# Optimization experiments

Hardware: AMD Instinct MI355X
Metric: run time of the kernel (lower is better)

The kernel has to match this reference:

```python
import jax, jax.numpy as jnp
import numpy as np

DIM = 256
HEADS = 8
HEAD_DIM = DIM // HEADS
SCALE = HEAD_DIM ** -0.5
B, H, W = 4, 48, 48


def setup_inputs() -> dict:
    key = jax.random.key(0)
    ks = jax.random.split(key, 10)
    s = 1.0 / np.sqrt(DIM)
    return {
        "img_features": jax.random.normal(ks[0], (B, DIM, H, W), jnp.float32),
        "radar_features": jax.random.normal(ks[1], (B, DIM, H, W), jnp.float32),
        "uncertainty_mask": jax.random.uniform(ks[2], (B, 1, H, W), jnp.float32),
        "Wq_img": jax.random.normal(ks[3], (DIM, DIM), jnp.float32) * s,
        "Wkv_radar": jax.random.normal(ks[4], (DIM, 2 * DIM), jnp.float32) * s,
        "Wq_radar": jax.random.normal(ks[5], (DIM, DIM), jnp.float32) * s,
        "Wkv_img": jax.random.normal(ks[6], (DIM, 2 * DIM), jnp.float32) * s,
        "Wp_img": jax.random.normal(ks[7], (DIM, DIM), jnp.float32) * s,
        "bp_img": jnp.zeros((DIM,), jnp.float32),
        "Wp_radar": jax.random.normal(ks[8], (DIM, DIM), jnp.float32) * s,
        "bp_radar": jnp.zeros((DIM,), jnp.float32),
    }


def _heads(x, b, n):
    # (B, N, C) -> (B, heads, N, head_dim)
    return x.reshape(b, n, HEADS, HEAD_DIM).transpose(0, 2, 1, 3)


def _cross_attn(q_seq, kv_seq, Wq, Wkv, uw=None):
    b, n, c = q_seq.shape
    q = _heads(q_seq @ Wq, b, n)                      # (B,h,N,d)
    kv = (kv_seq @ Wkv).reshape(b, n, 2, HEADS, HEAD_DIM)
    k = kv[:, :, 0].transpose(0, 2, 1, 3)             # (B,h,N,d)
    v = kv[:, :, 1].transpose(0, 2, 1, 3)
    scores = jnp.einsum("bhnd,bhmd->bhnm", q, k) * SCALE
    if uw is not None:
        scores = scores * uw                          # (B,1,N,1) broadcast
    p = jax.nn.softmax(scores, axis=-1)
    out = jnp.einsum("bhnm,bhmd->bhnd", p, v)
    return out.transpose(0, 2, 1, 3).reshape(b, n, c)


def reference(img_features, radar_features, uncertainty_mask,
              Wq_img, Wkv_radar, Wq_radar, Wkv_img,
              Wp_img, bp_img, Wp_radar, bp_radar):
    b, c, h, w = img_features.shape
    n = h * w
    img_seq = img_features.reshape(b, c, n).transpose(0, 2, 1)    # (B,N,C)
    radar_seq = radar_features.reshape(b, c, n).transpose(0, 2, 1)

    # uncertainty weight: (B,1,N,1), scales query rows before softmax
    u_seq = uncertainty_mask.reshape(b, 1, n).transpose(0, 2, 1)  # (B,N,1)
    uw = (1.0 / (u_seq + 1e-6))[:, None, :, :]

    img_att = _cross_attn(img_seq, radar_seq, Wq_img, Wkv_radar, uw)
    img_att = img_att @ Wp_img + bp_img

    radar_att = _cross_attn(radar_seq, img_seq, Wq_radar, Wkv_img, None)
    radar_att = radar_att @ Wp_radar + bp_radar

    img_out = img_att.transpose(0, 2, 1).reshape(b, c, h, w)
    radar_out = radar_att.transpose(0, 2, 1).reshape(b, c, h, w)
    return img_out, radar_out
```

## Files before the change

kernel.cpp:

```cpp
#include <hip/hip_runtime.h>
#include <math.h>

#define NB    4
#define CDIM  256
#define NSEQ  2304
#define NHEAD 8
#define HD    32
#define QSCALE (0.17677669529663687f * 1.4426950408889634f)
#define INV2048 4.8828125e-4f
#define FIXMAX 12.0f

typedef _Float16 f16;
typedef _Float16 f16x8 __attribute__((ext_vector_type(8)));
typedef _Float16 f16x4 __attribute__((ext_vector_type(4)));
typedef _Float16 f16x2 __attribute__((ext_vector_type(2)));
typedef float    f32x4 __attribute__((ext_vector_type(4)));
typedef float    f32x16 __attribute__((ext_vector_type(16)));
typedef unsigned u32x4 __attribute__((ext_vector_type(4)));

__device__ __forceinline__ float fast_exp2(float x) {
#if __has_builtin(__builtin_amdgcn_exp2f)
  return __builtin_amdgcn_exp2f(x);
#else
  return exp2f(x);
#endif
}

__device__ __forceinline__ unsigned pkrtz(float a, float b) {
#if __has_builtin(__builtin_amdgcn_cvt_pkrtz)
  auto h = __builtin_amdgcn_cvt_pkrtz(a, b);
  return __builtin_bit_cast(unsigned, h);
#else
  f16x2 h; h[0] = (f16)a; h[1] = (f16)b;
  return __builtin_bit_cast(unsigned, h);
#endif
}

__device__ __forceinline__ void gload_lds16(const f16* g, f16* l) {
  __builtin_amdgcn_global_load_lds(
      (const __attribute__((address_space(1))) void*)g,
      (__attribute__((address_space(3))) void*)l, 16, 0, 0);
}

__device__ __forceinline__ void plswap(unsigned &a, unsigned &b) {
#if __has_builtin(__builtin_amdgcn_permlane32_swap)
  auto r = __builtin_amdgcn_permlane32_swap(a, b, false, false);
  a = r[0]; b = r[1];
#else
  asm("v_permlane32_swap_b32 %0, %1" : "+v"(a), "+v"(b));
#endif
}

__device__ __forceinline__ float cross_fmax(float v) {
  unsigned a = __builtin_bit_cast(unsigned, v), b;
  asm("v_mov_b32 %0, %1" : "=v"(b) : "v"(a));
  plswap(a, b);
  return fmaxf(__builtin_bit_cast(float, a), __builtin_bit_cast(float, b));
}
__device__ __forceinline__ float cross_add(float v) {
  unsigned a = __builtin_bit_cast(unsigned, v), b;
  asm("v_mov_b32 %0, %1" : "=v"(b) : "v"(a));
  plswap(a, b);
  return __builtin_bit_cast(float, a) + __builtin_bit_cast(float, b);
}

__global__ __launch_bounds__(256) void prep_split(
    const float* __restrict__ X0, const float* __restrict__ X1,
    const float* __restrict__ Wq0, const float* __restrict__ Wkv0,
    const float* __restrict__ Wp0, const float* __restrict__ Wq1,
    const float* __restrict__ Wkv1, const float* __restrict__ Wp1,
    f16* __restrict__ X16h, f16* __restrict__ X16l,
    f16* __restrict__ WTh, f16* __restrict__ WTl)
{
  __shared__ float Ls[64][65];
  const int t = threadIdx.x;
  const int id = blockIdx.x;

  const float* in; int incols, c0, col0; size_t obase; f16 *oh, *ol;
  float scale = 1.f;
  if (id < 1152) {
    int mb = id / 144, rem = id % 144;
    int ct = rem / 36, nt = rem % 36;
    int mod = mb >> 2, b = mb & 3;
    in = (mod ? X1 : X0) + (size_t)b * 256 * NSEQ;
    incols = NSEQ; c0 = ct * 64; col0 = nt * 64;
    obase = (size_t)mb * NSEQ + col0;
    oh = X16h; ol = X16l;
  } else {
    int wid = id - 1152;
    int mod = wid >> 6, r = wid & 63;
    int jt, ct2, rowoff;
    if (r < 16) {
      in = mod ? Wq1 : Wq0; incols = 256; jt = r >> 2; ct2 = r & 3;
      rowoff = 0; scale = QSCALE;
    } else if (r < 48) {
      int rr = r - 16;
      in = mod ? Wkv1 : Wkv0; incols = 512; jt = rr >> 2; ct2 = rr & 3;
      rowoff = 256;
    } else {
      int rr = r - 48;
      in = mod ? Wp1 : Wp0; incols = 256; jt = rr >> 2; ct2 = rr & 3;
      rowoff = 768;
    }
    c0 = ct2 * 64; col0 = jt * 64;
    obase = (size_t)mod * 1024 + rowoff + col0;
    oh = WTh; ol = WTl;
  }

#pragma unroll
  for (int i = 0; i < 4; ++i) {
    int cl = (t >> 4) + i * 16;
    int n4 = (t & 15) * 4;
    *(float4*)&Ls[cl][n4] =
        *(const float4*)(in + (size_t)(c0 + cl) * incols + col0 + n4);
  }
  __syncthreads();
#pragma unroll
  for (int i = 0; i < 4; ++i) {
    int ll = (t >> 4) + i * 16;
    int c4 = (t & 15) * 4;
    f16x4 hv, lv;
#pragma unroll
    for (int j = 0; j < 4; ++j) {
      float v = Ls[c4 + j][ll] * scale;
      f16 hh = (f16)v;
      hv[j] = hh;
      lv[j] = (f16)((v - (float)hh) * 2048.0f);
    }
    size_t o = (obase + ll) * 256 + c0 + c4;
    *(f16x4*)(oh + o) = hv;
    *(f16x4*)(ol + o) = lv;
  }
}

__global__ __launch_bounds__(256) void proj_qkv_mfma(
    const f16* __restrict__ X16h, const f16* __restrict__ X16l,
    const f16* __restrict__ WTh, const f16* __restrict__ WTl,
    f16* __restrict__ Qh, f16* __restrict__ Ql,
    f16* __restrict__ Kh, f16* __restrict__ Kl, f16* __restrict__ Vt)
{
  __shared__ f16 WhS[128][32];
  __shared__ f16 WlS[128][32];
  __shared__ f16 XhS[64][32];
  __shared__ f16 XlS[64][32];

  const int zz = blockIdx.z, mod = zz >> 2, b = zz & 3;
  const int n0 = blockIdx.y * 64, j0 = blockIdx.x * 128;
  const int t = threadIdx.x;
  const int wave = t >> 6, lane = t & 63;
  const int col = lane & 15, quad = lane >> 4;
  const int rsub = lane >> 2, seg8 = (lane & 3) * 8;

  const bool need_lo = (j0 < 256) ? (mod == 0)
                     : (j0 < 512) ? (mod == 1) : false;

  const size_t wbase = (size_t)mod * 1024 + j0;
  const size_t xbase = ((size_t)(mod * NB + b) * NSEQ + n0) * 256;

  f32x4 am[2][4], ac[2][4];
#pragma unroll
  for (int s = 0; s < 2; ++s)
#pragma unroll
    for (int tt = 0; tt < 4; ++tt) {
      am[s][tt] = (f32x4){0.f, 0.f, 0.f, 0.f};
      ac[s][tt] = (f32x4){0.f, 0.f, 0.f, 0.f};
    }

  for (int c0 = 0; c0 < 256; c0 += 32) {
    __syncthreads();
    {
      const f16* gw = WTh + (wbase + wave * 32 + rsub) * 256 + c0 + seg8;
      gload_lds16(gw,            &WhS[wave * 32][0]);
      gload_lds16(gw + 16 * 256, &WhS[wave * 32 + 16][0]);
      const f16* gx = X16h + xbase + (size_t)(wave * 16 + rsub) * 256 + c0 + seg8;
      gload_lds16(gx, &XhS[wave * 16][0]);
      if (need_lo) {
        const f16* gwl = WTl + (wbase + wave * 32 + rsub) * 256 + c0 + seg8;
        gload_lds16(gwl,            &WlS[wave * 32][0]);
        gload_lds16(gwl + 16 * 256, &WlS[wave * 32 + 16][0]);
        const f16* gxl = X16l + xbase + (size_t)(wave * 16 + rsub) * 256 + c0 + seg8;
        gload_lds16(gxl, &XlS[wave * 16][0]);
      }
    }
    __syncthreads();

    f16x8 Ah0 = *(const f16x8*)&WhS[wave * 32 + col][quad * 8];
    f16x8 Ah1 = *(const f16x8*)&WhS[wave * 32 + 16 + col][quad * 8];
    if (need_lo) {
      f16x8 Al0 = *(const f16x8*)&WlS[wave * 32 + col][quad * 8];
      f16x8 Al1 = *(const f16x8*)&WlS[wave * 32 + 16 + col][quad * 8];
#pragma unroll
      for (int tt = 0; tt < 4; ++tt) {
        f16x8 Bh = *(const f16x8*)&XhS[tt * 16 + col][quad * 8];
        f16x8 Bl = *(const f16x8*)&XlS[tt * 16 + col][quad * 8];
        am[0][tt] = __builtin_amdgcn_mfma_f32_16x16x32_f16(Ah0, Bh, am[0][tt], 0, 0, 0);
        ac[0][tt] = __builtin_amdgcn_mfma_f32_16x16x32_f16(Ah0, Bl, ac[0][tt], 0, 0, 0);
        ac[0][tt] = __builtin_amdgcn_mfma_f32_16x16x32_f16(Al0, Bh, ac[0][tt], 0, 0, 0);
        am[1][tt] = __builtin_amdgcn_mfma_f32_16x16x32_f16(Ah1, Bh, am[1][tt], 0, 0, 0);
        ac[1][tt] = __builtin_amdgcn_mfma_f32_16x16x32_f16(Ah1, Bl, ac[1][tt], 0, 0, 0);
        ac[1][tt] = __builtin_amdgcn_mfma_f32_16x16x32_f16(Al1, Bh, ac[1][tt], 0, 0, 0);
      }
    } else {
#pragma unroll
      for (int tt = 0; tt < 4; ++tt) {
        f16x8 Bh = *(const f16x8*)&XhS[tt * 16 + col][quad * 8];
        am[0][tt] = __builtin_amdgcn_mfma_f32_16x16x32_f16(Ah0, Bh, am[0][tt], 0, 0, 0);
        am[1][tt] = __builtin_amdgcn_mfma_f32_16x16x32_f16(Ah1, Bh, am[1][tt], 0, 0, 0);
      }
    }
  }

#pragma unroll
  for (int s = 0; s < 2; ++s) {
    const int jq = j0 + wave * 32 + s * 16 + quad * 4;
#pragma unroll
    for (int tt = 0; tt < 4; ++tt) {
      const int n = n0 + tt * 16 + col;
      float v[4];
#pragma unroll
      for (int r = 0; r < 4; ++r)
        v[r] = need_lo ? fmaf(ac[s][tt][r], INV2048, am[s][tt][r])
                       : am[s][tt][r];
      if (jq < 256) {
        f16x4 hv, lv;
#pragma unroll
        for (int r = 0; r < 4; ++r) {
          f16 hh = (f16)v[r]; hv[r] = hh;
          lv[r] = (f16)(v[r] - (float)hh);
        }
        *(f16x4*)(Qh + ((size_t)(mod * NB + b) * NSEQ + n) * 256 + jq) = hv;
        if (mod == 0)
          *(f16x4*)(Ql + ((size_t)b * NSEQ + n) * 256 + jq) = lv;
      } else if (jq < 512) {
        f16x4 hv, lv;
#pragma unroll
        for (int r = 0; r < 4; ++r) {
          f16 hh = (f16)v[r]; hv[r] = hh;
          lv[r] = (f16)(v[r] - (float)hh);
        }
        *(f16x4*)(Kh + ((size_t)(mod * NB + b) * NSEQ + n) * 256 + (jq - 256)) = hv;
        if (mod == 1)
          *(f16x4*)(Kl + ((size_t)b * NSEQ + n) * 256 + (jq - 256)) = lv;
      } else {
#pragma unroll
        for (int r = 0; r < 4; ++r)
          Vt[((size_t)(mod * NB + b) * 256 + (jq - 512 + r)) * NSEQ + n] = (f16)v[r];
      }
    }
  }
}

__global__ __launch_bounds__(256, 3) void attn_mfma(
    const f16* __restrict__ Qh, const f16* __restrict__ Ql,
    const f16* __restrict__ Kh, const f16* __restrict__ Kl,
    const f16* __restrict__ Vt, const float* __restrict__ U,
    f16* __restrict__ A16)
{
  __shared__ __align__(16) f16 KhS[64][40];
  __shared__ __align__(16) f16 KlS[64][40];
  __shared__ __align__(16) f16 VtS[32][72];

  const int branch = blockIdx.x;
  const int bh = blockIdx.y, b = bh >> 3, h = bh & 7;
  const int tid = threadIdx.x;
  const int wave = tid >> 6, lane = tid & 63;
  const int c32 = lane & 31, hi = lane >> 5;
  const int qr = blockIdx.z * 128 + wave * 32 + c32;

  unsigned da = (lane < 32) ? 1u : 2u;
  unsigned db = (lane < 32) ? 3u : 4u;
  plswap(da, db);
  const bool varA = (__builtin_amdgcn_readfirstlane((int)da) == 1);

  const int qmod = branch, kmod = 1 - branch;
  const size_t qbase = (size_t)(qmod * NB + b) * NSEQ * 256;
  const size_t kbase = (size_t)(kmod * NB + b) * NSEQ;
  const size_t kbaseL = (size_t)b * NSEQ;
  const size_t vbase = (size_t)(kmod * NB + b) * 256;

  f16x8 bqh[2], bql[2] = {};
  bqh[0] = *(const f16x8*)(Qh + qbase + (size_t)qr * 256 + h * HD + hi * 8);
  bqh[1] = *(const f16x8*)(Qh + qbase + (size_t)qr * 256 + h * HD + 16 + hi * 8);
  float uw = 1.0f;
  if (branch == 0) {
    const size_t qbaseL = (size_t)b * NSEQ * 256;
    bql[0] = *(const f16x8*)(Ql + qbaseL + (size_t)qr * 256 + h * HD + hi * 8);
    bql[1] = *(const f16x8*)(Ql + qbaseL + (size_t)qr * 256 + h * HD + 16 + hi * 8);
    uw = 1.0f / (U[b * NSEQ + qr] + 1e-6f);
  }

  float m = -1e30f, l = 0.f;
  f32x16 oc;
#pragma unroll
  for (int r = 0; r < 16; ++r) oc[r] = 0.f;
  f32x16 z16;
#pragma unroll
  for (int r = 0; r < 16; ++r) z16[r] = 0.f;

  const int krow = tid >> 2, kseg = (tid & 3) * 8;
  const int vrow = tid >> 3, vseg = (tid & 7) * 8;

  f16x8 pkh = *(const f16x8*)(Kh + (kbase + krow) * 256 + h * HD + kseg);
  f16x8 pkl = {};
  if (branch == 0)
    pkl = *(const f16x8*)(Kl + (kbaseL + krow) * 256 + h * HD + kseg);
  f16x8 pv = *(const f16x8*)(Vt + (vbase + h * HD + vrow) * NSEQ + vseg);

  for (int k0 = 0; k0 < NSEQ; k0 += 64) {
    __syncthreads();
    *(f16x8*)&KhS[krow][kseg] = pkh;
    if (branch == 0) *(f16x8*)&KlS[krow][kseg] = pkl;
    *(f16x8*)&VtS[vrow][vseg] = pv;
    __syncthreads();

    const int kn = (k0 + 64 < NSEQ) ? k0 + 64 : 0;
    pkh = *(const f16x8*)(Kh + (kbase + kn + krow) * 256 + h * HD + kseg);
    if (branch == 0)
      pkl = *(const f16x8*)(Kl + (kbaseL + kn + krow) * 256 + h * HD + kseg);
    pv = *(const f16x8*)(Vt + (vbase + h * HD + vrow) * NSEQ + kn + vseg);

    float p[2][16];
#pragma unroll
    for (int kt = 0; kt < 2; ++kt) {
      f32x16 acc;
      if (branch == 0) {
        f16x8 ah0 = *(const f16x8*)&KhS[kt * 32 + c32][hi * 8];
        f16x8 ah1 = *(const f16x8*)&KhS[kt * 32 + c32][16 + hi * 8];
        f16x8 al0 = *(const f16x8*)&KlS[kt * 32 + c32][hi * 8];
        f16x8 al1 = *(const f16x8*)&KlS[kt * 32 + c32][16 + hi * 8];
        acc = __builtin_amdgcn_mfma_f32_32x32x16_f16(ah0, bql[0], z16, 0, 0, 0);
        acc = __builtin_amdgcn_mfma_f32_32x32x16_f16(al0, bqh[0], acc, 0, 0, 0);
        acc = __builtin_amdgcn_mfma_f32_32x32x16_f16(ah1, bql[1], acc, 0, 0, 0);
        acc = __builtin_amdgcn_mfma_f32_32x32x16_f16(al1, bqh[1], acc, 0, 0, 0);
        acc = __builtin_amdgcn_mfma_f32_32x32x16_f16(ah0, bqh[0], acc, 0, 0, 0);
        acc = __builtin_amdgcn_mfma_f32_32x32x16_f16(ah1, bqh[1], acc, 0, 0, 0);
      } else {
        f16x8 ah0 = *(const f16x8*)&KhS[kt * 32 + c32][hi * 8];
        f16x8 ah1 = *(const f16x8*)&KhS[kt * 32 + c32][16 + hi * 8];
        acc = __builtin_amdgcn_mfma_f32_32x32x16_f16(ah0, bqh[0], z16, 0, 0, 0);
        acc = __builtin_amdgcn_mfma_f32_32x32x16_f16(ah1, bqh[1], acc, 0, 0, 0);
      }
#pragma unroll
      for (int r = 0; r < 16; ++r) p[kt][r] = acc[r];
    }

    if (branch == 0) {
      float t8[8];
#pragma unroll
      for (int i = 0; i < 8; ++i)
        t8[i] = fmaxf(fmaxf(fmaxf(p[0][i], p[0][i + 8]), p[1][i]), p[1][i + 8]);
#pragma unroll
      for (int s = 4; s > 0; s >>= 1)
#pragma unroll
        for (int i = 0; i < s; ++i) t8[i] = fmaxf(t8[i], t8[i + s]);
      float cmax = cross_fmax(t8[0] * uw);
      const bool nore = __all(cmax <= m);
      const float mn = nore ? m : fmaxf(m, cmax);
      float sA = 0.f, sB = 0.f;
#pragma unroll
      for (int kt = 0; kt < 2; ++kt)
#pragma unroll
        for (int r = 0; r < 16; r += 2) {
          float eA = fast_exp2(fmaf(p[kt][r],     uw, -mn));
          float eB = fast_exp2(fmaf(p[kt][r + 1], uw, -mn));
          p[kt][r] = eA; p[kt][r + 1] = eB;
          sA += eA; sB += eB;
        }
      if (nore) {
        l += sA + sB;
      } else {
        const float alpha = fast_exp2(m - mn);
        m = mn;
        l = fmaf(l, alpha, sA + sB);
#pragma unroll
        for (int r = 0; r < 16; ++r) oc[r] *= alpha;
      }
    } else {
      float sA = 0.f, sB = 0.f;
#pragma unroll
      for (int kt = 0; kt < 2; ++kt)
#pragma unroll
        for (int r = 0; r < 16; r += 2) {
          float eA = fast_exp2(p[kt][r]     - FIXMAX);
          float eB = fast_exp2(p[kt][r + 1] - FIXMAX);
          p[kt][r] = eA; p[kt][r + 1] = eB;
          sA += eA; sB += eB;
        }
      l += sA + sB;
    }

    unsigned pk[2][4][2];
#pragma unroll
    for (int kt = 0; kt < 2; ++kt)
#pragma unroll
      for (int Q = 0; Q < 4; ++Q) {
        pk[kt][Q][0] = pkrtz(p[kt][4 * Q],     p[kt][4 * Q + 1]);
        pk[kt][Q][1] = pkrtz(p[kt][4 * Q + 2], p[kt][4 * Q + 3]);
      }

#pragma unroll
    for (int km = 0; km < 4; ++km) {
      const int kt = km >> 1, Qb = (km & 1) * 2;
      unsigned w0 = pk[kt][Qb][0],     w1 = pk[kt][Qb][1];
      unsigned w2 = pk[kt][Qb + 1][0], w3 = pk[kt][Qb + 1][1];
      if (varA) { plswap(w0, w2); plswap(w1, w3); }
      else      { plswap(w2, w0); plswap(w3, w1); }
      u32x4 uv = {w0, w1, w2, w3};
      f16x8 bp = __builtin_bit_cast(f16x8, uv);
      f16x8 av = *(const f16x8*)&VtS[c32][km * 16 + hi * 8];
      oc = __builtin_amdgcn_mfma_f32_32x32x16_f16(av, bp, oc, 0, 0, 0);
    }
  }

  l = cross_add(l);

  const float iv = 1.0f / l;
  f16* d0 = A16 + (((size_t)(branch * NB + b) * NSEQ) + qr) * 256 + h * HD + hi * 4;
#pragma unroll
  for (int g = 0; g < 4; ++g) {
    f16x4 o;
#pragma unroll
    for (int r = 0; r < 4; ++r) o[r] = (f16)(oc[4 * g + r] * iv);
    *(f16x4*)(d0 + 8 * g) = o;
  }
}

__global__ __launch_bounds__(256) void proj_out_mfma(
    const f16* __restrict__ A16, const f16* __restrict__ WTh,
    const f16* __restrict__ WTl, const float* __restrict__ bp0,
    const float* __restrict__ bp1, float* __restrict__ O)
{
  __shared__ f16 WhS[128][32];
  __shared__ f16 WlS[128][32];
  __shared__ f16 AS[64][32];

  const int zz = blockIdx.z, mod = zz >> 2, b = zz & 3;
  const int n0 = blockIdx.y * 64, j0 = blockIdx.x * 128;
  const int t = threadIdx.x;
  const int wave = t >> 6, lane = t & 63;
  const int col = lane & 15, quad = lane >> 4;
  const int rsub = lane >> 2, seg8 = (lane & 3) * 8;

  const size_t wbase = (size_t)mod * 1024 + 768 + j0;
  const size_t abase = ((size_t)(mod * NB + b) * NSEQ + n0) * 256;

  f32x4 am[2][4], ac[2][4];
#pragma unroll
  for (int s = 0; s < 2; ++s)
#pragma unroll
    for (int tt = 0; tt < 4; ++tt) {
      am[s][tt] = (f32x4){0.f, 0.f, 0.f, 0.f};
      ac[s][tt] = (f32x4){0.f, 0.f, 0.f, 0.f};
    }

  for (int c0 = 0; c0 < 256; c0 += 32) {
    __syncthreads();
    {
      const f16* gw = WTh + (wbase + wave * 32 + rsub) * 256 + c0 + seg8;
      gload_lds16(gw,            &WhS[wave * 32][0]);
      gload_lds16(gw + 16 * 256, &WhS[wave * 32 + 16][0]);
      const f16* gwl = WTl + (wbase + wave * 32 + rsub) * 256 + c0 + seg8;
      gload_lds16(gwl,            &WlS[wave * 32][0]);
      gload_lds16(gwl + 16 * 256, &WlS[wave * 32 + 16][0]);
      const f16* ga = A16 + abase + (size_t)(wave * 16 + rsub) * 256 + c0 + seg8;
      gload_lds16(ga, &AS[wave * 16][0]);
    }
    __syncthreads();

    f16x8 Ah0 = *(const f16x8*)&WhS[wave * 32 + col][quad * 8];
    f16x8 Al0 = *(const f16x8*)&WlS[wave * 32 + col][quad * 8];
    f16x8 Ah1 = *(const f16x8*)&WhS[wave * 32 + 16 + col][quad * 8];
    f16x8 Al1 = *(const f16x8*)&WlS[wave * 32 + 16 + col][quad * 8];
#pragma unroll
    for (int tt = 0; tt < 4; ++tt) {
      f16x8 Bh = *(const f16x8*)&AS[tt * 16 + col][quad * 8];
      am[0][tt] = __builtin_amdgcn_mfma_f32_16x16x32_f16(Ah0, Bh, am[0][tt], 0, 0, 0);
      ac[0][tt] = __builtin_amdgcn_mfma_f32_16x16x32_f16(Al0, Bh, ac[0][tt], 0, 0, 0);
      am[1][tt] = __builtin_amdgcn_mfma_f32_16x16x32_f16(Ah1, Bh, am[1][tt], 0, 0, 0);
      ac[1][tt] = __builtin_amdgcn_mfma_f32_16x16x32_f16(Al1, Bh, ac[1][tt], 0, 0, 0);
    }
  }

  const float* bp = mod ? bp1 : bp0;
  float* Ob = O + (size_t)(mod * NB + b) * CDIM * NSEQ;
#pragma unroll
  for (int s = 0; s < 2; ++s) {
    const int jq = j0 + wave * 32 + s * 16 + quad * 4;
    const float4 bias = *(const float4*)(bp + jq);
    const float bias_r[4] = {bias.x, bias.y, bias.z, bias.w};
#pragma unroll
    for (int tt = 0; tt < 4; ++tt) {
      const int n = n0 + tt * 16 + col;
#pragma unroll
      for (int r = 0; r < 4; ++r) {
        float v = fmaf(ac[s][tt][r], INV2048, am[s][tt][r]) + bias_r[r];
        Ob[(size_t)(jq + r) * NSEQ + n] = v;
      }
    }
  }
}

extern "C" void kernel_launch(void* const* d_in, const int* in_sizes, int n_in,
                              void* d_out, int out_size, void* d_ws, size_t ws_size,
                              hipStream_t stream) {
  (void)in_sizes; (void)n_in; (void)out_size; (void)ws_size;
  const float* img     = (const float*)d_in[0];
  const float* rad     = (const float*)d_in[1];
  const float* U       = (const float*)d_in[2];
  const float* Wq_img  = (const float*)d_in[3];
  const float* Wkv_rad = (const float*)d_in[4];
  const float* Wq_rad  = (const float*)d_in[5];
  const float* Wkv_img = (const float*)d_in[6];
  const float* Wp_img  = (const float*)d_in[7];
  const float* bp_img  = (const float*)d_in[8];
  const float* Wp_rad  = (const float*)d_in[9];
  const float* bp_rad  = (const float*)d_in[10];
  float* out = (float*)d_out;

  const size_t NE = (size_t)2 * NB * NSEQ * 256;
  const size_t WE = (size_t)2 * 1024 * 256;
  f16* X16h = (f16*)d_ws;
  f16* X16l = X16h + NE;
  f16* WTh  = X16l + NE;
  f16* WTl  = WTh + WE;
  f16* Qh   = WTl + WE;
  f16* Ql   = Qh + NE;
  f16* Kh   = Ql + NE / 2;
  f16* Kl   = Kh + NE;
  f16* Vt   = Kl + NE / 2;
  f16* A16  = Vt + NE;

  prep_split<<<dim3(1280), 256, 0, stream>>>(
      img, rad, Wq_img, Wkv_img, Wp_img, Wq_rad, Wkv_rad, Wp_rad,
      X16h, X16l, WTh, WTl);

  dim3 gp(6, 36, 2 * NB);
  proj_qkv_mfma<<<gp, 256, 0, stream>>>(X16h, X16l, WTh, WTl,
                                        Qh, Ql, Kh, Kl, Vt);

  dim3 ga(2, NB * NHEAD, NSEQ / 128);
  attn_mfma<<<ga, 256, 0, stream>>>(Qh, Ql, Kh, Kl, Vt, U, A16);

  dim3 go(2, 36, 2 * NB);
  proj_out_mfma<<<go, 256, 0, stream>>>(A16, WTh, WTl, bp_img, bp_rad, out);
}
```

Measured before the change: 258.9 us.

## Split attention over two key halves and merge partials in a combine kernel

New measurement: 262.3 us. Within noise of the previous version (+1.3%).

```diff
diff --git a/kernel.cpp b/kernel.cpp
--- a/kernel.cpp
+++ b/kernel.cpp
@@ -254,7 +254,7 @@
     const f16* __restrict__ Qh, const f16* __restrict__ Ql,
     const f16* __restrict__ Kh, const f16* __restrict__ Kl,
     const f16* __restrict__ Vt, const float* __restrict__ U,
-    f16* __restrict__ A16)
+    f16* __restrict__ A16, f16* __restrict__ OP1, float* __restrict__ ML)
 {
   __shared__ __align__(16) f16 KhS[64][40];
   __shared__ __align__(16) f16 KlS[64][40];
@@ -262,10 +262,12 @@
 
   const int branch = blockIdx.x;
   const int bh = blockIdx.y, b = bh >> 3, h = bh & 7;
+  const int ks = blockIdx.z & 1, qt = blockIdx.z >> 1;
   const int tid = threadIdx.x;
   const int wave = tid >> 6, lane = tid & 63;
   const int c32 = lane & 31, hi = lane >> 5;
-  const int qr = blockIdx.z * 128 + wave * 32 + c32;
+  const int qr = qt * 128 + wave * 32 + c32;
+  const int kbeg = ks * (NSEQ / 2);
 
   unsigned da = (lane < 32) ? 1u : 2u;
   unsigned db = (lane < 32) ? 3u : 4u;
@@ -300,20 +302,20 @@
   const int krow = tid >> 2, kseg = (tid & 3) * 8;
   const int vrow = tid >> 3, vseg = (tid & 7) * 8;
 
-  f16x8 pkh = *(const f16x8*)(Kh + (kbase + krow) * 256 + h * HD + kseg);
+  f16x8 pkh = *(const f16x8*)(Kh + (kbase + kbeg + krow) * 256 + h * HD + kseg);
   f16x8 pkl = {};
   if (branch == 0)
-    pkl = *(const f16x8*)(Kl + (kbaseL + krow) * 256 + h * HD + kseg);
-  f16x8 pv = *(const f16x8*)(Vt + (vbase + h * HD + vrow) * NSEQ + vseg);
-
-  for (int k0 = 0; k0 < NSEQ; k0 += 64) {
+    pkl = *(const f16x8*)(Kl + (kbaseL + kbeg + krow) * 256 + h * HD + kseg);
+  f16x8 pv = *(const f16x8*)(Vt + (vbase + h * HD + vrow) * NSEQ + kbeg + vseg);
+
+  for (int k0 = kbeg; k0 < kbeg + NSEQ / 2; k0 += 64) {
     __syncthreads();
     *(f16x8*)&KhS[krow][kseg] = pkh;
     if (branch == 0) *(f16x8*)&KlS[krow][kseg] = pkl;
     *(f16x8*)&VtS[vrow][vseg] = pv;
     __syncthreads();
 
-    const int kn = (k0 + 64 < NSEQ) ? k0 + 64 : 0;
+    const int kn = (k0 + 64 < kbeg + NSEQ / 2) ? k0 + 64 : kbeg;
     pkh = *(const f16x8*)(Kh + (kbase + kn + krow) * 256 + h * HD + kseg);
     if (branch == 0)
       pkl = *(const f16x8*)(Kl + (kbaseL + kn + krow) * 256 + h * HD + kseg);
@@ -414,14 +416,50 @@
 
   l = cross_add(l);
 
-  const float iv = 1.0f / l;
-  f16* d0 = A16 + (((size_t)(branch * NB + b) * NSEQ) + qr) * 256 + h * HD + hi * 4;
+  f16* outp = (ks ? OP1 : A16)
+            + (((size_t)(branch * NB + b) * NSEQ) + qr) * 256 + h * HD + hi * 4;
 #pragma unroll
   for (int g = 0; g < 4; ++g) {
     f16x4 o;
 #pragma unroll
-    for (int r = 0; r < 4; ++r) o[r] = (f16)(oc[4 * g + r] * iv);
-    *(f16x4*)(d0 + 8 * g) = o;
+    for (int r = 0; r < 4; ++r) o[r] = (f16)oc[4 * g + r];
+    *(f16x4*)(outp + 8 * g) = o;
+  }
+  if (hi == 0) {
+    const int sl = (branch * NB + b) * NHEAD + h;
+    float2 mlv;
+    mlv.x = (branch == 0) ? m : FIXMAX;
+    mlv.y = l;
+    *(float2*)(ML + ((size_t)sl * NSEQ + qr) * 4 + ks * 2) = mlv;
+  }
+}
+
+__global__ __launch_bounds__(256) void attn_combine(
+    const f16* __restrict__ OP1, const float* __restrict__ ML,
+    f16* __restrict__ A16)
+{
+  const int s = blockIdx.y;
+  const int q = blockIdx.x * 256 + threadIdx.x;
+  const int brb = s >> 3, h = s & 7;
+  const size_t row = (size_t)brb * NSEQ + q;
+
+  const float4 ml = *(const float4*)(ML + ((size_t)s * NSEQ + q) * 4);
+  const float mt = fmaxf(ml.x, ml.z);
+  const float a0 = fast_exp2(ml.x - mt);
+  const float a1 = fast_exp2(ml.z - mt);
+  const float iv = 1.0f / fmaf(a0, ml.y, a1 * ml.w);
+
+  f16* pa = A16 + row * 256 + h * HD;
+  const f16* pb = OP1 + row * 256 + h * HD;
+#pragma unroll
+  for (int i = 0; i < 4; ++i) {
+    f16x8 v0 = *(const f16x8*)(pa + i * 8);
+    f16x8 v1 = *(const f16x8*)(pb + i * 8);
+    f16x8 o;
+#pragma unroll
+    for (int j = 0; j < 8; ++j)
+      o[j] = (f16)((a0 * (float)v0[j] + a1 * (float)v1[j]) * iv);
+    *(f16x8*)(pa + i * 8) = o;
   }
 }
 
@@ -529,6 +567,8 @@
   f16* Kl   = Kh + NE;
   f16* Vt   = Kl + NE / 2;
   f16* A16  = Vt + NE;
+  f16*   OP1 = X16h;
+  float* ML  = (float*)X16l;
 
   prep_split<<<dim3(1280), 256, 0, stream>>>(
       img, rad, Wq_img, Wkv_img, Wp_img, Wq_rad, Wkv_rad, Wp_rad,
@@ -538,8 +578,11 @@
   proj_qkv_mfma<<<gp, 256, 0, stream>>>(X16h, X16l, WTh, WTl,
                                         Qh, Ql, Kh, Kl, Vt);
 
-  dim3 ga(2, NB * NHEAD, NSEQ / 128);
-  attn_mfma<<<ga, 256, 0, stream>>>(Qh, Ql, Kh, Kl, Vt, U, A16);
+  dim3 ga(2, NB * NHEAD, (NSEQ / 128) * 2);
+  attn_mfma<<<ga, 256, 0, stream>>>(Qh, Ql, Kh, Kl, Vt, U, A16, OP1, ML);
+
+  dim3 gc(NSEQ / 256, 2 * NB * NHEAD);
+  attn_combine<<<gc, 256, 0, stream>>>(OP1, ML, A16);
 
   dim3 go(2, 36, 2 * NB);
   proj_out_mfma<<<go, 256, 0, stream>>>(A16, WTh, WTl, bp_img, bp_rad, out);
```

## Split attention KV range across two wave groups and merge partial softmax

Applied to the files above, without the earlier changes.

Measured after the change: 287.6 us. +11.1%, slower.

```diff
diff --git a/kernel.cpp b/kernel.cpp
--- a/kernel.cpp
+++ b/kernel.cpp
@@ -250,22 +250,25 @@
   }
 }
 
-__global__ __launch_bounds__(256, 3) void attn_mfma(
+__global__ __launch_bounds__(512) void attn_mfma(
     const f16* __restrict__ Qh, const f16* __restrict__ Ql,
     const f16* __restrict__ Kh, const f16* __restrict__ Kl,
     const f16* __restrict__ Vt, const float* __restrict__ U,
     f16* __restrict__ A16)
 {
-  __shared__ __align__(16) f16 KhS[64][40];
-  __shared__ __align__(16) f16 KlS[64][40];
-  __shared__ __align__(16) f16 VtS[32][72];
+  __shared__ __align__(16) f16 KhS[2][64][40];
+  __shared__ __align__(16) f16 KlS[2][64][40];
+  __shared__ __align__(16) f16 VtS[2][32][72];
 
   const int branch = blockIdx.x;
   const int bh = blockIdx.y, b = bh >> 3, h = bh & 7;
   const int tid = threadIdx.x;
   const int wave = tid >> 6, lane = tid & 63;
+  const int kh = wave >> 2;
+  const int w4 = wave & 3;
   const int c32 = lane & 31, hi = lane >> 5;
-  const int qr = blockIdx.z * 128 + wave * 32 + c32;
+  const int qr = blockIdx.z * 128 + w4 * 32 + c32;
+  const int kbeg = kh * (NSEQ / 2);
 
   unsigned da = (lane < 32) ? 1u : 2u;
   unsigned db = (lane < 32) ? 3u : 4u;
@@ -297,23 +300,25 @@
 #pragma unroll
   for (int r = 0; r < 16; ++r) z16[r] = 0.f;
 
-  const int krow = tid >> 2, kseg = (tid & 3) * 8;
-  const int vrow = tid >> 3, vseg = (tid & 7) * 8;
-
-  f16x8 pkh = *(const f16x8*)(Kh + (kbase + krow) * 256 + h * HD + kseg);
+  const int t2 = tid & 255;
+  const int krow = t2 >> 2, kseg = (t2 & 3) * 8;
+  const int vrow = t2 >> 3, vseg = (t2 & 7) * 8;
+
+  f16x8 pkh = *(const f16x8*)(Kh + (kbase + kbeg + krow) * 256 + h * HD + kseg);
   f16x8 pkl = {};
   if (branch == 0)
-    pkl = *(const f16x8*)(Kl + (kbaseL + krow) * 256 + h * HD + kseg);
-  f16x8 pv = *(const f16x8*)(Vt + (vbase + h * HD + vrow) * NSEQ + vseg);
-
-  for (int k0 = 0; k0 < NSEQ; k0 += 64) {
+    pkl = *(const f16x8*)(Kl + (kbaseL + kbeg + krow) * 256 + h * HD + kseg);
+  f16x8 pv = *(const f16x8*)(Vt + (vbase + h * HD + vrow) * NSEQ + kbeg + vseg);
+
+  for (int c = 0; c < NSEQ / 128; ++c) {
+    const int k0 = kbeg + c * 64;
     __syncthreads();
-    *(f16x8*)&KhS[krow][kseg] = pkh;
-    if (branch == 0) *(f16x8*)&KlS[krow][kseg] = pkl;
-    *(f16x8*)&VtS[vrow][vseg] = pv;
+    *(f16x8*)&KhS[kh][krow][kseg] = pkh;
+    if (branch == 0) *(f16x8*)&KlS[kh][krow][kseg] = pkl;
+    *(f16x8*)&VtS[kh][vrow][vseg] = pv;
     __syncthreads();
 
-    const int kn = (k0 + 64 < NSEQ) ? k0 + 64 : 0;
+    const int kn = (c + 1 < NSEQ / 128) ? k0 + 64 : kbeg;
     pkh = *(const f16x8*)(Kh + (kbase + kn + krow) * 256 + h * HD + kseg);
     if (branch == 0)
       pkl = *(const f16x8*)(Kl + (kbaseL + kn + krow) * 256 + h * HD + kseg);
@@ -324,10 +329,10 @@
     for (int kt = 0; kt < 2; ++kt) {
       f32x16 acc;
       if (branch == 0) {
-        f16x8 ah0 = *(const f16x8*)&KhS[kt * 32 + c32][hi * 8];
-        f16x8 ah1 = *(const f16x8*)&KhS[kt * 32 + c32][16 + hi * 8];
-        f16x8 al0 = *(const f16x8*)&KlS[kt * 32 + c32][hi * 8];
-        f16x8 al1 = *(const f16x8*)&KlS[kt * 32 + c32][16 + hi * 8];
+        f16x8 ah0 = *(const f16x8*)&KhS[kh][kt * 32 + c32][hi * 8];
+        f16x8 ah1 = *(const f16x8*)&KhS[kh][kt * 32 + c32][16 + hi * 8];
+        f16x8 al0 = *(const f16x8*)&KlS[kh][kt * 32 + c32][hi * 8];
+        f16x8 al1 = *(const f16x8*)&KlS[kh][kt * 32 + c32][16 + hi * 8];
         acc = __builtin_amdgcn_mfma_f32_32x32x16_f16(ah0, bql[0], z16, 0, 0, 0);
         acc = __builtin_amdgcn_mfma_f32_32x32x16_f16(al0, bqh[0], acc, 0, 0, 0);
         acc = __builtin_amdgcn_mfma_f32_32x32x16_f16(ah1, bql[1], acc, 0, 0, 0);
@@ -335,8 +340,8 @@
         acc = __builtin_amdgcn_mfma_f32_32x32x16_f16(ah0, bqh[0], acc, 0, 0, 0);
         acc = __builtin_amdgcn_mfma_f32_32x32x16_f16(ah1, bqh[1], acc, 0, 0, 0);
       } else {
-        f16x8 ah0 = *(const f16x8*)&KhS[kt * 32 + c32][hi * 8];
-        f16x8 ah1 = *(const f16x8*)&KhS[kt * 32 + c32][16 + hi * 8];
+        f16x8 ah0 = *(const f16x8*)&KhS[kh][kt * 32 + c32][hi * 8];
+        f16x8 ah1 = *(const f16x8*)&KhS[kh][kt * 32 + c32][16 + hi * 8];
         acc = __builtin_amdgcn_mfma_f32_32x32x16_f16(ah0, bqh[0], z16, 0, 0, 0);
         acc = __builtin_amdgcn_mfma_f32_32x32x16_f16(ah1, bqh[1], acc, 0, 0, 0);
       }
@@ -407,21 +412,47 @@
       else      { plswap(w2, w0); plswap(w3, w1); }
       u32x4 uv = {w0, w1, w2, w3};
       f16x8 bp = __builtin_bit_cast(f16x8, uv);
-      f16x8 av = *(const f16x8*)&VtS[c32][km * 16 + hi * 8];
+      f16x8 av = *(const f16x8*)&VtS[kh][c32][km * 16 + hi * 8];
       oc = __builtin_amdgcn_mfma_f32_32x32x16_f16(av, bp, oc, 0, 0, 0);
     }
   }
 
   l = cross_add(l);
 
-  const float iv = 1.0f / l;
-  f16* d0 = A16 + (((size_t)(branch * NB + b) * NSEQ) + qr) * 256 + h * HD + hi * 4;
-#pragma unroll
-  for (int g = 0; g < 4; ++g) {
-    f16x4 o;
-#pragma unroll
-    for (int r = 0; r < 4; ++r) o[r] = (f16)(oc[4 * g + r] * iv);
-    *(f16x4*)(d0 + 8 * g) = o;
+  __syncthreads();
+  float* MrgA = (float*)&KhS[0][0][0];
+  float* MrgB = (float*)&KlS[0][0][0];
+  const int sl = w4 * 64 + lane;
+  if (kh == 1) {
+    float* sa = MrgA + sl * 10;
+#pragma unroll
+    for (int r = 0; r < 8; ++r) sa[r] = oc[r];
+    sa[8] = m; sa[9] = l;
+    float* sb = MrgB + sl * 8;
+#pragma unroll
+    for (int r = 0; r < 8; ++r) sb[r] = oc[8 + r];
+  }
+  __syncthreads();
+  if (kh == 0) {
+    const float* sa = MrgA + sl * 10;
+    const float* sb = MrgB + sl * 8;
+    const float m1 = sa[8], l1 = sa[9];
+    const float mt = fmaxf(m, m1);
+    const float a0 = fast_exp2(m - mt);
+    const float a1 = fast_exp2(m1 - mt);
+    const float iv = 1.0f / fmaf(a0, l, a1 * l1);
+
+    f16* d0 = A16 + (((size_t)(branch * NB + b) * NSEQ) + qr) * 256 + h * HD + hi * 4;
+#pragma unroll
+    for (int g = 0; g < 4; ++g) {
+      f16x4 o;
+#pragma unroll
+      for (int r = 0; r < 4; ++r) {
+        const float other = (g < 2) ? sa[4 * g + r] : sb[4 * (g - 2) + r];
+        o[r] = (f16)((a0 * oc[4 * g + r] + a1 * other) * iv);
+      }
+      *(f16x4*)(d0 + 8 * g) = o;
+    }
   }
 }
 
@@ -539,7 +570,7 @@
                                         Qh, Ql, Kh, Kl, Vt);
 
   dim3 ga(2, NB * NHEAD, NSEQ / 128);
-  attn_mfma<<<ga, 256, 0, stream>>>(Qh, Ql, Kh, Kl, Vt, U, A16);
+  attn_mfma<<<ga, 512, 0, stream>>>(Qh, Ql, Kh, Kl, Vt, U, A16);
 
   dim3 go(2, 36, 2 * NB);
   proj_out_mfma<<<go, 256, 0, stream>>>(A16, WTh, WTl, bp_img, bp_rad, out);
```
